# Kernel optimization log

Measured on AMD Instinct MI355X. Metric: run time of the kernel, lower is better.

## Reference

```python
import jax, jax.numpy as jnp
import numpy as np
import math

N, E, D, H, L = 50000, 800000, 256, 8, 8
DK = D // H
DFF = 4 * D


def _layernorm(h, g, b, eps=1e-5):
    m = jnp.mean(h, axis=-1, keepdims=True)
    v = jnp.mean((h - m) ** 2, axis=-1, keepdims=True)
    return (h - m) * jax.lax.rsqrt(v + eps) * g + b


def setup_inputs() -> dict:
    key = jax.random.key(0)
    ks = jax.random.split(key, 16)
    s = 1.0 / math.sqrt(D)
    x = jax.random.normal(ks[0], (N, D), dtype=jnp.float32)
    # every node gets >=1 in-edge so z > 0 everywhere (as in real connected graphs)
    edge_src = jax.random.randint(ks[1], (E,), 0, N, dtype=jnp.int32)
    edge_dst = jnp.concatenate([
        jnp.arange(N, dtype=jnp.int32),
        jax.random.randint(ks[2], (E - N,), 0, N, dtype=jnp.int32),
    ])
    return {
        "x": x,
        "edge_src": edge_src,
        "edge_dst": edge_dst,
        "Wq": jax.random.normal(ks[3], (L, D, D), dtype=jnp.float32) * s,
        "bq": jnp.zeros((L, D), dtype=jnp.float32),
        "Wk": jax.random.normal(ks[4], (L, D, D), dtype=jnp.float32) * s,
        "Wv": jax.random.normal(ks[5], (L, D, D), dtype=jnp.float32) * s,
        "Wo": jax.random.normal(ks[6], (L, D, D), dtype=jnp.float32) * s,
        "bo": jnp.zeros((L, D), dtype=jnp.float32),
        "ln1_g": jnp.ones((L, D), dtype=jnp.float32),
        "ln1_b": jnp.zeros((L, D), dtype=jnp.float32),
        "W1": jax.random.normal(ks[7], (L, D, DFF), dtype=jnp.float32) * s,
        "b1": jnp.zeros((L, DFF), dtype=jnp.float32),
        "W2": jax.random.normal(ks[8], (L, DFF, D), dtype=jnp.float32) * (1.0 / math.sqrt(DFF)),
        "b2": jnp.zeros((L, D), dtype=jnp.float32),
        "ln2_g": jnp.ones((L, D), dtype=jnp.float32),
        "ln2_b": jnp.zeros((L, D), dtype=jnp.float32),
    }


def _layer(x, src, dst, Wq, bq, Wk, Wv, Wo, bo, g1, b1n, W1, b1, W2, b2, g2, b2n):
    n = x.shape[0]
    q = (x @ Wq + bq).reshape(n, H, DK)
    k = (x @ Wk).reshape(n, H, DK)
    v = (x @ Wv).reshape(n, H, DK)
    # edge score: src_dot_dst('k','q') -> [E, H]
    score = jnp.einsum('ehd,ehd->eh', k[src], q[dst])
    # scaled_exp: exp(clamp(score / sqrt(d_k), -5, 5))
    score = jnp.exp(jnp.clip(score / math.sqrt(DK), -5.0, 5.0))
    # u_mul_e + sum aggregation -> wv [N, H, DK]; copy_edge + sum -> z [N, H]
    msg = v[src] * score[:, :, None]
    wv = jax.ops.segment_sum(msg, dst, num_segments=n)
    z = jax.ops.segment_sum(score, dst, num_segments=n)
    o = (wv / z[:, :, None]).reshape(n, D)
    h = _layernorm(x + o @ Wo + bo, g1, b1n)
    # FFN with residual + layernorm
    ff = jax.nn.relu(h @ W1 + b1) @ W2 + b2
    return _layernorm(h + ff, g2, b2n)


def reference(x, edge_src, edge_dst, Wq, bq, Wk, Wv, Wo, bo, ln1_g, ln1_b,
              W1, b1, W2, b2, ln2_g, ln2_b):
    for i in range(L):
        x = _layer(x, edge_src, edge_dst, Wq[i], bq[i], Wk[i], Wv[i], Wo[i],
                   bo[i], ln1_g[i], ln1_b[i], W1[i], b1[i], W2[i], b2[i],
                   ln2_g[i], ln2_b[i])
    return x
```

## Files before the change

kernel.cpp:

```cpp
#include <hip/hip_runtime.h>
#include <cstdint>
#include <cstddef>

#define D 256
#define H 8
#define DFF 1024

typedef short s16x8 __attribute__((ext_vector_type(8)));
typedef float f32x4 __attribute__((ext_vector_type(4)));

static inline int cdiv(int a, int b) { return (a + b - 1) / b; }

__device__ inline uint16_t f2bf(float x) {
    unsigned u = __float_as_uint(x);
    u += 0x7FFFu + ((u >> 16) & 1u);
    return (uint16_t)(u >> 16);
}
__device__ inline float bf2f(uint16_t h) {
    return __uint_as_float(((unsigned)h) << 16);
}

__device__ inline void gload_lds16(const void* g, void* l) {
    __builtin_amdgcn_global_load_lds(
        (const __attribute__((address_space(1))) void*)g,
        (__attribute__((address_space(3))) void*)l, 16, 0, 0);
}

__global__ __launch_bounds__(256) void zero_int_kernel(int* __restrict__ p, int count)
{
    int i = blockIdx.x * blockDim.x + threadIdx.x;
    if (i < count) p[i] = 0;
}

__global__ __launch_bounds__(256) void count_deg_kernel(
    const int* __restrict__ edst, int* __restrict__ deg, int E)
{
    int e = blockIdx.x * blockDim.x + threadIdx.x;
    if (e < E) atomicAdd(&deg[edst[e]], 1);
}

__global__ __launch_bounds__(256) void block_sum_kernel(
    const int* __restrict__ deg, int* __restrict__ bsum, int N)
{
    int t = threadIdx.x;
    int gid = blockIdx.x * 256 + t;
    int val = (gid < N) ? deg[gid] : 0;
    #pragma unroll
    for (int o = 1; o < 64; o <<= 1) val += __shfl_xor(val, o);
    __shared__ int r[4];
    if ((t & 63) == 0) r[t >> 6] = val;
    __syncthreads();
    if (t == 0) bsum[blockIdx.x] = r[0] + r[1] + r[2] + r[3];
}

__global__ __launch_bounds__(256) void scan_bsum_kernel(int* __restrict__ bsum, int nb)
{
    __shared__ int tmp[256];
    int t = threadIdx.x;
    int val = (t < nb) ? bsum[t] : 0;
    tmp[t] = val;
    __syncthreads();
    for (int off = 1; off < 256; off <<= 1) {
        int add = (t >= off) ? tmp[t - off] : 0;
        __syncthreads();
        tmp[t] += add;
        __syncthreads();
    }
    if (t < nb) bsum[t] = tmp[t] - val;
}

__global__ __launch_bounds__(256) void scan_write_kernel(
    const int* __restrict__ deg, const int* __restrict__ bsum,
    int* __restrict__ rowptr, int* __restrict__ cursor, int N)
{
    __shared__ int tmp[256];
    int t = threadIdx.x;
    int gid = blockIdx.x * 256 + t;
    int val = (gid < N) ? deg[gid] : 0;
    tmp[t] = val;
    __syncthreads();
    for (int off = 1; off < 256; off <<= 1) {
        int add = (t >= off) ? tmp[t - off] : 0;
        __syncthreads();
        tmp[t] += add;
        __syncthreads();
    }
    int excl = tmp[t] - val + bsum[blockIdx.x];
    if (gid < N) { rowptr[gid] = excl; cursor[gid] = excl; }
    if (gid == N - 1) rowptr[N] = excl + val;
}

__global__ __launch_bounds__(256) void fill_csr_kernel(
    const int* __restrict__ esrc, const int* __restrict__ edst,
    int* __restrict__ cursor, int* __restrict__ csr_src, int E)
{
    int e = blockIdx.x * blockDim.x + threadIdx.x;
    if (e < E) {
        int pos = atomicAdd(&cursor[edst[e]], 1);
        csr_src[pos] = esrc[e];
    }
}

__global__ __launch_bounds__(256) void transpose_cast_kernel(
    const float* __restrict__ in, uint16_t* __restrict__ out,
    int R, int C, size_t inLS, size_t outLS)
{
    __shared__ float t[32][33];
    in  += blockIdx.z * inLS;
    out += blockIdx.z * outLS;
    int c0 = blockIdx.x * 32, r0 = blockIdx.y * 32;
    int tx = threadIdx.x, ty = threadIdx.y;
    #pragma unroll
    for (int i = 0; i < 4; ++i)
        t[ty + i * 8][tx] = in[(size_t)(r0 + ty + i * 8) * C + c0 + tx];
    __syncthreads();
    #pragma unroll
    for (int i = 0; i < 4; ++i)
        out[(size_t)(c0 + ty + i * 8) * R + r0 + tx] = f2bf(t[tx][ty + i * 8]);
}

__global__ __launch_bounds__(256) void cast_f32_bf16_kernel(
    const float* __restrict__ in, uint16_t* __restrict__ out, int n4)
{
    int i = blockIdx.x * blockDim.x + threadIdx.x;
    if (i >= n4) return;
    float4 f = ((const float4*)in)[i];
    uint16_t o0 = f2bf(f.x), o1 = f2bf(f.y), o2 = f2bf(f.z), o3 = f2bf(f.w);
    uint2 pk;
    pk.x = (unsigned)o0 | ((unsigned)o1 << 16);
    pk.y = (unsigned)o2 | ((unsigned)o3 << 16);
    ((uint2*)out)[i] = pk;
}

__global__ __launch_bounds__(256) void build_qkv_bias_kernel(
    const float* __restrict__ bq, float* __restrict__ qb, int total)
{
    int i = blockIdx.x * blockDim.x + threadIdx.x;
    if (i >= total) return;
    int l = i / 768, c = i - l * 768;
    qb[i] = (c < 256) ? bq[l * 256 + c] : 0.f;
}

__global__ __launch_bounds__(256) void gemm_bf16_kernel(
    const uint16_t* __restrict__ A, int lda, int M, int K,
    const uint16_t* __restrict__ BT, int Nc,
    const float* __restrict__ bias,
    uint16_t* __restrict__ Cb, int relu)
{
    __shared__ __align__(16) uint16_t As[128 * 32];
    __shared__ __align__(16) uint16_t Bs[128 * 32];

    const int tid  = threadIdx.x;
    const int lane = tid & 63;
    const int w    = tid >> 6;
    const int wr   = w >> 1, wc = w & 1;
    const int quad = lane >> 4;
    const int l15  = lane & 15;

    const int m0 = blockIdx.x * 128;
    const int n0 = blockIdx.y * 128;

    f32x4 acc[4][4] = {};

    const int jbase = w * 2;
    const int srow  = lane >> 2;
    const int skc   = (lane & 3) * 8;

    for (int k0 = 0; k0 < K; k0 += 32) {
        #pragma unroll
        for (int jj = 0; jj < 2; ++jj) {
            int j = jbase + jj;
            int r = j * 16 + srow;
            int gr = m0 + r; if (gr > M - 1) gr = M - 1;
            gload_lds16(A  + (size_t)gr * lda + k0 + skc, &As[j * 512]);
            gload_lds16(BT + (size_t)(n0 + r) * K + k0 + skc, &Bs[j * 512]);
        }
        __syncthreads();

        s16x8 af[4], bf[4];
        #pragma unroll
        for (int t = 0; t < 4; ++t) {
            af[t] = *(const s16x8*)&As[(wr * 64 + t * 16 + l15) * 32 + quad * 8];
            bf[t] = *(const s16x8*)&Bs[(wc * 64 + t * 16 + l15) * 32 + quad * 8];
        }
        #pragma unroll
        for (int i = 0; i < 4; ++i)
            #pragma unroll
            for (int jt = 0; jt < 4; ++jt)
                acc[i][jt] = __builtin_amdgcn_mfma_f32_16x16x32_bf16(
                    af[i], bf[jt], acc[i][jt], 0, 0, 0);
        __syncthreads();
    }

    float bv[4];
    #pragma unroll
    for (int jt = 0; jt < 4; ++jt)
        bv[jt] = bias ? bias[n0 + wc * 64 + jt * 16 + l15] : 0.f;

    #pragma unroll
    for (int i = 0; i < 4; ++i) {
        #pragma unroll
        for (int r = 0; r < 4; ++r) {
            int m = m0 + wr * 64 + i * 16 + quad * 4 + r;
            if (m >= M) continue;
            #pragma unroll
            for (int jt = 0; jt < 4; ++jt) {
                int n = n0 + wc * 64 + jt * 16 + l15;
                float val = acc[i][jt][r] + bv[jt];
                if (relu) val = fmaxf(val, 0.f);
                Cb[(size_t)m * Nc + n] = f2bf(val);
            }
        }
    }
}

__global__ __launch_bounds__(256) void gemm_ln_kernel(
    const uint16_t* __restrict__ A, int lda, int M, int K,
    const uint16_t* __restrict__ BT,
    const float* __restrict__ bias,
    const float* __restrict__ resid,
    const float* __restrict__ g, const float* __restrict__ b,
    float* __restrict__ Cf, uint16_t* __restrict__ Cb)
{
    __shared__ __align__(16) uint16_t As[64 * 32];
    __shared__ __align__(16) uint16_t Bs[256 * 32];
    __shared__ float sS[64][4];
    __shared__ float sQ[64][4];

    const int tid  = threadIdx.x;
    const int lane = tid & 63;
    const int w    = tid >> 6;
    const int quad = lane >> 4;
    const int l15  = lane & 15;

    const int m0 = blockIdx.x * 64;

    f32x4 acc[4][4] = {};

    for (int k0 = 0; k0 < K; k0 += 32) {
        {
            int slot = tid;
            int r = slot >> 2, kc = (slot & 3) * 8;
            int gr = m0 + r; if (gr > M - 1) gr = M - 1;
            gload_lds16(A + (size_t)gr * lda + k0 + kc, &As[slot * 8]);
        }
        #pragma unroll
        for (int i = 0; i < 4; ++i) {
            int slot = i * 256 + tid;
            int n = slot >> 2, kc = (slot & 3) * 8;
            gload_lds16(BT + (size_t)n * K + k0 + kc, &Bs[slot * 8]);
        }
        __syncthreads();

        s16x8 af[4], bf[4];
        #pragma unroll
        for (int t = 0; t < 4; ++t) {
            af[t] = *(const s16x8*)&As[(t * 16 + l15) * 32 + quad * 8];
            bf[t] = *(const s16x8*)&Bs[(w * 64 + t * 16 + l15) * 32 + quad * 8];
        }
        #pragma unroll
        for (int i = 0; i < 4; ++i)
            #pragma unroll
            for (int jt = 0; jt < 4; ++jt)
                acc[i][jt] = __builtin_amdgcn_mfma_f32_16x16x32_bf16(
                    af[i], bf[jt], acc[i][jt], 0, 0, 0);
        __syncthreads();
    }

    float bv[4], gv[4], bbv[4];
    #pragma unroll
    for (int jt = 0; jt < 4; ++jt) {
        int n = w * 64 + jt * 16 + l15;
        bv[jt]  = bias[n];
        gv[jt]  = g[n];
        bbv[jt] = b[n];
    }

    #pragma unroll
    for (int i = 0; i < 4; ++i) {
        #pragma unroll
        for (int r = 0; r < 4; ++r) {
            int ml = i * 16 + quad * 4 + r;
            int m  = m0 + ml;
            bool valid = (m < M);
            float s = 0.f, s2 = 0.f;
            #pragma unroll
            for (int jt = 0; jt < 4; ++jt) {
                int n = w * 64 + jt * 16 + l15;
                float val = acc[i][jt][r] + bv[jt];
                if (valid) val += resid[(size_t)m * 256 + n];
                acc[i][jt][r] = val;
                s += val;
                s2 += val * val;
            }
            #pragma unroll
            for (int o = 1; o < 16; o <<= 1) {
                s  += __shfl_xor(s, o);
                s2 += __shfl_xor(s2, o);
            }
            if (l15 == 0) { sS[ml][w] = s; sQ[ml][w] = s2; }
        }
    }
    __syncthreads();

    #pragma unroll
    for (int i = 0; i < 4; ++i) {
        #pragma unroll
        for (int r = 0; r < 4; ++r) {
            int ml = i * 16 + quad * 4 + r;
            int m  = m0 + ml;
            if (m >= M) continue;
            float s  = sS[ml][0] + sS[ml][1] + sS[ml][2] + sS[ml][3];
            float s2 = sQ[ml][0] + sQ[ml][1] + sQ[ml][2] + sQ[ml][3];
            float mean = s * (1.f / 256.f);
            float var  = s2 * (1.f / 256.f) - mean * mean;
            float rstd = rsqrtf(var + 1e-5f);
            #pragma unroll
            for (int jt = 0; jt < 4; ++jt) {
                int n = w * 64 + jt * 16 + l15;
                float out = (acc[i][jt][r] - mean) * rstd * gv[jt] + bbv[jt];
                Cf[(size_t)m * 256 + n] = out;
                if (Cb) Cb[(size_t)m * 256 + n] = f2bf(out);
            }
        }
    }
}

__global__ __launch_bounds__(256) void node_attn_kernel(
    uint16_t* __restrict__ qkv,
    const int* __restrict__ rowptr, const int* __restrict__ csr_src, int N)
{
    int node = (blockIdx.x * blockDim.x + threadIdx.x) >> 6;
    int lane = threadIdx.x & 63;
    if (node >= N) return;

    uint16_t* qp = qkv + (size_t)node * 768 + lane * 4;
    uint2 qu = *(const uint2*)qp;
    float q0 = bf2f((uint16_t)(qu.x & 0xFFFF)), q1 = bf2f((uint16_t)(qu.x >> 16));
    float q2 = bf2f((uint16_t)(qu.y & 0xFFFF)), q3 = bf2f((uint16_t)(qu.y >> 16));

    float a0 = 0.f, a1 = 0.f, a2 = 0.f, a3 = 0.f, zacc = 0.f;
    const float inv_sqrt_dk = 0.17677669529663687f;

    int beg = rowptr[node], end = rowptr[node + 1];
    int i = beg;
    for (; i + 1 < end; i += 2) {
        int s0 = csr_src[i], s1 = csr_src[i + 1];
        const uint16_t* b0 = qkv + (size_t)s0 * 768;
        const uint16_t* b1 = qkv + (size_t)s1 * 768;
        uint2 ku0 = *(const uint2*)(b0 + 256 + lane * 4);
        uint2 ku1 = *(const uint2*)(b1 + 256 + lane * 4);
        uint2 vu0 = *(const uint2*)(b0 + 512 + lane * 4);
        uint2 vu1 = *(const uint2*)(b1 + 512 + lane * 4);

        float p0 = bf2f((uint16_t)(ku0.x & 0xFFFF)) * q0
                 + bf2f((uint16_t)(ku0.x >> 16))   * q1
                 + bf2f((uint16_t)(ku0.y & 0xFFFF)) * q2
                 + bf2f((uint16_t)(ku0.y >> 16))   * q3;
        float p1 = bf2f((uint16_t)(ku1.x & 0xFFFF)) * q0
                 + bf2f((uint16_t)(ku1.x >> 16))   * q1
                 + bf2f((uint16_t)(ku1.y & 0xFFFF)) * q2
                 + bf2f((uint16_t)(ku1.y >> 16))   * q3;
        p0 += __shfl_xor(p0, 1); p1 += __shfl_xor(p1, 1);
        p0 += __shfl_xor(p0, 2); p1 += __shfl_xor(p1, 2);
        p0 += __shfl_xor(p0, 4); p1 += __shfl_xor(p1, 4);
        float sc0 = __expf(fminf(fmaxf(p0 * inv_sqrt_dk, -5.f), 5.f));
        float sc1 = __expf(fminf(fmaxf(p1 * inv_sqrt_dk, -5.f), 5.f));

        a0 += bf2f((uint16_t)(vu0.x & 0xFFFF)) * sc0;
        a1 += bf2f((uint16_t)(vu0.x >> 16))   * sc0;
        a2 += bf2f((uint16_t)(vu0.y & 0xFFFF)) * sc0;
        a3 += bf2f((uint16_t)(vu0.y >> 16))   * sc0;
        zacc += sc0;
        a0 += bf2f((uint16_t)(vu1.x & 0xFFFF)) * sc1;
        a1 += bf2f((uint16_t)(vu1.x >> 16))   * sc1;
        a2 += bf2f((uint16_t)(vu1.y & 0xFFFF)) * sc1;
        a3 += bf2f((uint16_t)(vu1.y >> 16))   * sc1;
        zacc += sc1;
    }
    if (i < end) {
        int s = csr_src[i];
        const uint16_t* base = qkv + (size_t)s * 768;
        uint2 ku = *(const uint2*)(base + 256 + lane * 4);
        float p = bf2f((uint16_t)(ku.x & 0xFFFF)) * q0
                + bf2f((uint16_t)(ku.x >> 16))   * q1
                + bf2f((uint16_t)(ku.y & 0xFFFF)) * q2
                + bf2f((uint16_t)(ku.y >> 16))   * q3;
        p += __shfl_xor(p, 1);
        p += __shfl_xor(p, 2);
        p += __shfl_xor(p, 4);
        float sc = __expf(fminf(fmaxf(p * inv_sqrt_dk, -5.f), 5.f));
        uint2 vu = *(const uint2*)(base + 512 + lane * 4);
        a0 += bf2f((uint16_t)(vu.x & 0xFFFF)) * sc;
        a1 += bf2f((uint16_t)(vu.x >> 16))   * sc;
        a2 += bf2f((uint16_t)(vu.y & 0xFFFF)) * sc;
        a3 += bf2f((uint16_t)(vu.y >> 16))   * sc;
        zacc += sc;
    }
    float inv = 1.f / zacc;
    uint2 pk;
    pk.x = (unsigned)f2bf(a0 * inv) | ((unsigned)f2bf(a1 * inv) << 16);
    pk.y = (unsigned)f2bf(a2 * inv) | ((unsigned)f2bf(a3 * inv) << 16);
    *(uint2*)qp = pk;
}

extern "C" void kernel_launch(void* const* d_in, const int* in_sizes, int n_in,
                              void* d_out, int out_size, void* d_ws, size_t ws_size,
                              hipStream_t stream)
{
    const float* x0   = (const float*)d_in[0];
    const int* esrc   = (const int*)d_in[1];
    const int* edst   = (const int*)d_in[2];
    const float* Wq   = (const float*)d_in[3];
    const float* bq   = (const float*)d_in[4];
    const float* Wk   = (const float*)d_in[5];
    const float* Wv   = (const float*)d_in[6];
    const float* Wo   = (const float*)d_in[7];
    const float* bo   = (const float*)d_in[8];
    const float* ln1g = (const float*)d_in[9];
    const float* ln1b = (const float*)d_in[10];
    const float* W1   = (const float*)d_in[11];
    const float* b1   = (const float*)d_in[12];
    const float* W2   = (const float*)d_in[13];
    const float* b2   = (const float*)d_in[14];
    const float* ln2g = (const float*)d_in[15];
    const float* ln2b = (const float*)d_in[16];

    const int N = in_sizes[0] / D;
    const int E = in_sizes[1];
    const int L = in_sizes[3] / (D * D);
    const size_t ND = (size_t)N * D;

    char* p = (char*)d_ws;
    float* bufX = (float*)p;         p += ND * 4;
    uint16_t* xb  = (uint16_t*)p;
    uint16_t* t1  = xb;              p += ND * 2;
    uint16_t* qkv = (uint16_t*)p;    p += (size_t)N * 768 * 2;
    uint16_t* hb  = (uint16_t*)p;    p += ND * 2;
    uint16_t* BTqkv = (uint16_t*)p;  p += (size_t)L * 768 * 256 * 2;
    uint16_t* BTo   = (uint16_t*)p;  p += (size_t)L * 256 * 256 * 2;
    uint16_t* BT1   = (uint16_t*)p;  p += (size_t)L * 1024 * 256 * 2;
    uint16_t* BT2   = (uint16_t*)p;  p += (size_t)L * 256 * 1024 * 2;
    float* qbias    = (float*)p;     p += (size_t)L * 768 * 4;
    int* rowptr  = (int*)p;          p += (size_t)(N + 1) * 4;
    int* cursor  = (int*)p;          p += (size_t)N * 4;
    int* deg     = cursor;
    int* csr_src = (int*)p;          p += (size_t)E * 4;
    int* bsum    = (int*)p;

    const int nb = cdiv(N, 256);
    dim3 blk(256);
    int edgeBlocks = cdiv(E, 256);
    int nodeBlocks = cdiv(N, 4);

    dim3 tb(32, 8);
    transpose_cast_kernel<<<dim3(8, 8, L), tb, 0, stream>>>(Wq, BTqkv, 256, 256, (size_t)65536, (size_t)768 * 256);
    transpose_cast_kernel<<<dim3(8, 8, L), tb, 0, stream>>>(Wk, BTqkv + 256 * 256, 256, 256, (size_t)65536, (size_t)768 * 256);
    transpose_cast_kernel<<<dim3(8, 8, L), tb, 0, stream>>>(Wv, BTqkv + 512 * 256, 256, 256, (size_t)65536, (size_t)768 * 256);
    transpose_cast_kernel<<<dim3(8, 8, L), tb, 0, stream>>>(Wo, BTo, 256, 256, (size_t)65536, (size_t)65536);
    transpose_cast_kernel<<<dim3(32, 8, L), tb, 0, stream>>>(W1, BT1, 256, 1024, (size_t)262144, (size_t)262144);
    transpose_cast_kernel<<<dim3(8, 32, L), tb, 0, stream>>>(W2, BT2, 1024, 256, (size_t)262144, (size_t)262144);
    build_qkv_bias_kernel<<<cdiv(L * 768, 256), blk, 0, stream>>>(bq, qbias, L * 768);
    cast_f32_bf16_kernel<<<cdiv((int)(ND / 4), 256), blk, 0, stream>>>(x0, xb, (int)(ND / 4));

    zero_int_kernel<<<cdiv(N, 256), blk, 0, stream>>>(deg, N);
    count_deg_kernel<<<edgeBlocks, blk, 0, stream>>>(edst, deg, E);
    block_sum_kernel<<<nb, blk, 0, stream>>>(deg, bsum, N);
    scan_bsum_kernel<<<1, blk, 0, stream>>>(bsum, nb);
    scan_write_kernel<<<nb, blk, 0, stream>>>(deg, bsum, rowptr, cursor, N);
    fill_csr_kernel<<<edgeBlocks, blk, 0, stream>>>(esrc, edst, cursor, csr_src, E);

    const int Mt128 = cdiv(N, 128);
    const int Mt64  = cdiv(N, 64);
    dim3 gQKV(Mt128, 768 / 128);
    dim3 gF1(Mt128, 1024 / 128);
    dim3 gLN(Mt64, 1);

    for (int l = 0; l < L; ++l) {
        const uint16_t* BTqkv_l = BTqkv + (size_t)l * 768 * 256;
        const uint16_t* BTo_l   = BTo + (size_t)l * 65536;
        const uint16_t* BT1_l   = BT1 + (size_t)l * 262144;
        const uint16_t* BT2_l   = BT2 + (size_t)l * 262144;
        const float* xin_f = (l == 0) ? x0 : bufX;

        gemm_bf16_kernel<<<gQKV, blk, 0, stream>>>(xb, 256, N, 256, BTqkv_l, 768,
            qbias + (size_t)l * 768, qkv, 0);

        node_attn_kernel<<<nodeBlocks, blk, 0, stream>>>(qkv, rowptr, csr_src, N);

        gemm_ln_kernel<<<gLN, blk, 0, stream>>>(qkv, 768, N, 256, BTo_l,
            bo + (size_t)l * 256, xin_f, ln1g + (size_t)l * 256, ln1b + (size_t)l * 256,
            bufX, hb);

        gemm_bf16_kernel<<<gF1, blk, 0, stream>>>(hb, 256, N, 256, BT1_l, 1024,
            b1 + (size_t)l * 1024, t1, 1);

        float* fout = (l == L - 1) ? (float*)d_out : bufX;
        gemm_ln_kernel<<<gLN, blk, 0, stream>>>(t1, 1024, N, 1024, BT2_l,
            b2 + (size_t)l * 256, bufX, ln2g + (size_t)l * 256, ln2b + (size_t)l * 256,
            fout, (l == L - 1) ? nullptr : xb);

        xin_f = bufX;
    }
}
```

Before: 3.425 ms.

## Fuse FFN up/down GEMMs into one kernel and remap GEMM blocks per XCD

Adds a fused FFN kernel that, per 64-row tile, computes the relu(hW1+b1) intermediate in 128-column chunks held in LDS and immediately accumulates it into the W2 product, followed by the residual add and layernorm. This removes the global write and re-read of the N×1024 bf16 intermediate and one kernel launch per layer. In exchange, the shared A tile is reloaded for every chunk, there is no software pipelining, and each chunk has many syncthreads. It also remaps block indices in the generic GEMM so that consecutive tiles land on the same XCD, aiming for better L2 locality.

```diff
diff --git a/kernel.cpp b/kernel.cpp
--- a/kernel.cpp
+++ b/kernel.cpp
@@ -157,8 +157,16 @@
     const int quad = lane >> 4;
     const int l15  = lane & 15;
 
-    const int m0 = blockIdx.x * 128;
-    const int n0 = blockIdx.y * 128;
+    const int nwg = gridDim.x * gridDim.y;
+    const int lin = blockIdx.y * gridDim.x + blockIdx.x;
+    const int xcd = lin & 7, idx = lin >> 3;
+    const int q8 = nwg >> 3, r8 = nwg & 7;
+    const int lin2 = (xcd < r8 ? xcd * (q8 + 1) : r8 * (q8 + 1) + (xcd - r8) * q8) + idx;
+    const int mt = lin2 % gridDim.x;
+    const int nt = lin2 / gridDim.x;
+
+    const int m0 = mt * 128;
+    const int n0 = nt * 128;
 
     f32x4 acc[4][4] = {};
 
@@ -319,6 +327,168 @@
             for (int jt = 0; jt < 4; ++jt) {
                 int n = w * 64 + jt * 16 + l15;
                 float out = (acc[i][jt][r] - mean) * rstd * gv[jt] + bbv[jt];
+                Cf[(size_t)m * 256 + n] = out;
+                if (Cb) Cb[(size_t)m * 256 + n] = f2bf(out);
+            }
+        }
+    }
+}
+
+__global__ __launch_bounds__(256) void ffn_fused_kernel(
+    const uint16_t* __restrict__ A,
+    int M,
+    const uint16_t* __restrict__ BT1,
+    const float* __restrict__ b1,
+    const uint16_t* __restrict__ BT2,
+    const float* __restrict__ b2,
+    const float* __restrict__ resid,
+    const float* __restrict__ g, const float* __restrict__ b,
+    float* __restrict__ Cf, uint16_t* __restrict__ Cb)
+{
+    __shared__ __align__(16) uint16_t As[64 * 32];
+    __shared__ __align__(16) uint16_t Bs[256 * 32];
+    __shared__ __align__(16) uint16_t Ts[64 * 128];
+    __shared__ float sS[64][4];
+    __shared__ float sQ[64][4];
+
+    const int tid  = threadIdx.x;
+    const int lane = tid & 63;
+    const int w    = tid >> 6;
+    const int quad = lane >> 4;
+    const int l15  = lane & 15;
+    const int m0   = blockIdx.x * 64;
+
+    f32x4 acc2[4][4] = {};
+
+    for (int c = 0; c < 8; ++c) {
+        f32x4 acc1[4][2] = {};
+
+        for (int k0 = 0; k0 < 256; k0 += 32) {
+            {
+                int r = tid >> 2, kc = (tid & 3) * 8;
+                int gr = m0 + r; if (gr > M - 1) gr = M - 1;
+                gload_lds16(A + (size_t)gr * 256 + k0 + kc, &As[tid * 8]);
+            }
+            #pragma unroll
+            for (int i = 0; i < 2; ++i) {
+                int slot = i * 256 + tid;
+                int n = slot >> 2, kc = (slot & 3) * 8;
+                gload_lds16(BT1 + (size_t)(c * 128 + n) * 256 + k0 + kc, &Bs[slot * 8]);
+            }
+            __syncthreads();
+
+            s16x8 af[4], bf1[2];
+            #pragma unroll
+            for (int t = 0; t < 4; ++t)
+                af[t] = *(const s16x8*)&As[(t * 16 + l15) * 32 + quad * 8];
+            #pragma unroll
+            for (int jt = 0; jt < 2; ++jt)
+                bf1[jt] = *(const s16x8*)&Bs[(w * 32 + jt * 16 + l15) * 32 + quad * 8];
+            #pragma unroll
+            for (int i = 0; i < 4; ++i)
+                #pragma unroll
+                for (int jt = 0; jt < 2; ++jt)
+                    acc1[i][jt] = __builtin_amdgcn_mfma_f32_16x16x32_bf16(
+                        af[i], bf1[jt], acc1[i][jt], 0, 0, 0);
+            __syncthreads();
+        }
+
+        float bv1[2];
+        #pragma unroll
+        for (int jt = 0; jt < 2; ++jt)
+            bv1[jt] = b1[c * 128 + w * 32 + jt * 16 + l15];
+        #pragma unroll
+        for (int i = 0; i < 4; ++i)
+            #pragma unroll
+            for (int r = 0; r < 4; ++r) {
+                int ml = i * 16 + quad * 4 + r;
+                #pragma unroll
+                for (int jt = 0; jt < 2; ++jt) {
+                    float val = acc1[i][jt][r] + bv1[jt];
+                    val = fmaxf(val, 0.f);
+                    Ts[w * 2048 + ml * 32 + jt * 16 + l15] = f2bf(val);
+                }
+            }
+        __syncthreads();
+
+        for (int ts = 0; ts < 4; ++ts) {
+            #pragma unroll
+            for (int i = 0; i < 4; ++i) {
+                int slot = i * 256 + tid;
+                int n = slot >> 2, kc = (slot & 3) * 8;
+                gload_lds16(BT2 + (size_t)n * 1024 + c * 128 + ts * 32 + kc, &Bs[slot * 8]);
+            }
+            __syncthreads();
+
+            s16x8 af2[4], bf2[4];
+            #pragma unroll
+            for (int i = 0; i < 4; ++i)
+                af2[i] = *(const s16x8*)&Ts[ts * 2048 + (i * 16 + l15) * 32 + quad * 8];
+            #pragma unroll
+            for (int jt = 0; jt < 4; ++jt)
+                bf2[jt] = *(const s16x8*)&Bs[(w * 64 + jt * 16 + l15) * 32 + quad * 8];
+            #pragma unroll
+            for (int i = 0; i < 4; ++i)
+                #pragma unroll
+                for (int jt = 0; jt < 4; ++jt)
+                    acc2[i][jt] = __builtin_amdgcn_mfma_f32_16x16x32_bf16(
+                        af2[i], bf2[jt], acc2[i][jt], 0, 0, 0);
+            __syncthreads();
+        }
+    }
+
+    float bv[4], gv[4], bbv[4];
+    #pragma unroll
+    for (int jt = 0; jt < 4; ++jt) {
+        int n = w * 64 + jt * 16 + l15;
+        bv[jt]  = b2[n];
+        gv[jt]  = g[n];
+        bbv[jt] = b[n];
+    }
+
+    #pragma unroll
+    for (int i = 0; i < 4; ++i) {
+        #pragma unroll
+        for (int r = 0; r < 4; ++r) {
+            int ml = i * 16 + quad * 4 + r;
+            int m  = m0 + ml;
+            bool valid = (m < M);
+            float s = 0.f, s2 = 0.f;
+            #pragma unroll
+            for (int jt = 0; jt < 4; ++jt) {
+                int n = w * 64 + jt * 16 + l15;
+                float val = acc2[i][jt][r] + bv[jt];
+                if (valid) val += resid[(size_t)m * 256 + n];
+                acc2[i][jt][r] = val;
+                s += val;
+                s2 += val * val;
+            }
+            #pragma unroll
+            for (int o = 1; o < 16; o <<= 1) {
+                s  += __shfl_xor(s, o);
+                s2 += __shfl_xor(s2, o);
+            }
+            if (l15 == 0) { sS[ml][w] = s; sQ[ml][w] = s2; }
+        }
+    }
+    __syncthreads();
+
+    #pragma unroll
+    for (int i = 0; i < 4; ++i) {
+        #pragma unroll
+        for (int r = 0; r < 4; ++r) {
+            int ml = i * 16 + quad * 4 + r;
+            int m  = m0 + ml;
+            if (m >= M) continue;
+            float s  = sS[ml][0] + sS[ml][1] + sS[ml][2] + sS[ml][3];
+            float s2 = sQ[ml][0] + sQ[ml][1] + sQ[ml][2] + sQ[ml][3];
+            float mean = s * (1.f / 256.f);
+            float var  = s2 * (1.f / 256.f) - mean * mean;
+            float rstd = rsqrtf(var + 1e-5f);
+            #pragma unroll
+            for (int jt = 0; jt < 4; ++jt) {
+                int n = w * 64 + jt * 16 + l15;
+                float out = (acc2[i][jt][r] - mean) * rstd * gv[jt] + bbv[jt];
                 Cf[(size_t)m * 256 + n] = out;
                 if (Cb) Cb[(size_t)m * 256 + n] = f2bf(out);
             }
@@ -447,6 +617,7 @@
     int* deg     = cursor;
     int* csr_src = (int*)p;          p += (size_t)E * 4;
     int* bsum    = (int*)p;
+    (void)t1;
 
     const int nb = cdiv(N, 256);
     dim3 blk(256);
@@ -473,7 +644,6 @@
     const int Mt128 = cdiv(N, 128);
     const int Mt64  = cdiv(N, 64);
     dim3 gQKV(Mt128, 768 / 128);
-    dim3 gF1(Mt128, 1024 / 128);
     dim3 gLN(Mt64, 1);
 
     for (int l = 0; l < L; ++l) {
@@ -492,12 +662,10 @@
             bo + (size_t)l * 256, xin_f, ln1g + (size_t)l * 256, ln1b + (size_t)l * 256,
             bufX, hb);
 
-        gemm_bf16_kernel<<<gF1, blk, 0, stream>>>(hb, 256, N, 256, BT1_l, 1024,
-            b1 + (size_t)l * 1024, t1, 1);
-
         float* fout = (l == L - 1) ? (float*)d_out : bufX;
-        gemm_ln_kernel<<<gLN, blk, 0, stream>>>(t1, 1024, N, 1024, BT2_l,
-            b2 + (size_t)l * 256, bufX, ln2g + (size_t)l * 256, ln2b + (size_t)l * 256,
+        ffn_fused_kernel<<<gLN, blk, 0, stream>>>(hb, N, BT1_l,
+            b1 + (size_t)l * 1024, BT2_l, b2 + (size_t)l * 256, bufX,
+            ln2g + (size_t)l * 256, ln2b + (size_t)l * 256,
             fout, (l == L - 1) ? nullptr : xb);
 
         xin_f = bufX;
```

Result: faster. 3.316 ms (-3.2%).
